# Performance work log

Measured on AMD Instinct MI355X. Metric: run time of the kernel, lower is better.

The kernel has to match this reference:

```python
import jax, jax.numpy as jnp
import numpy as np

DIM = 512
HEADS = 8
DH = DIM // HEADS          # 64
SCALE = DH ** (-0.5)
B, H, W = 8, 64, 64        # N = 4096, H and W multiples of 8 -> exact adaptive pool
N = H * W
POOL = 8                   # AdaptiveAvgPool2d((8,8)) -> 64 pooled tokens


def setup_inputs() -> dict:
    key = jax.random.key(0)
    ks = jax.random.split(key, 6)
    return {
        "x": jax.random.normal(ks[0], (B, N, DIM), dtype=jnp.float32),
        "proj_w": jax.random.normal(ks[1], (DIM, DIM), dtype=jnp.float32) * (DIM ** -0.5),
        "step_rep": jax.random.normal(ks[2], (HEADS, 1, 1), dtype=jnp.float32),
        "step_x": jax.random.normal(ks[3], (HEADS, 1, 1), dtype=jnp.float32),
        "to_out_w": jax.random.normal(ks[4], (DIM, DIM), dtype=jnp.float32) * (DIM ** -0.5),
        "to_out_b": jax.random.normal(ks[5], (DIM,), dtype=jnp.float32),
    }


def reference(x, proj_w, step_rep, step_x, to_out_w, to_out_b):
    b, n, c = x.shape
    # proj (Linear, no bias): w = x @ proj_w.T
    w = jnp.einsum('bnc,dc->bnd', x, proj_w)                       # [B,N,C]
    # AdaptiveAvgPool2d to (8,8): exact block mean since H,W % 8 == 0
    bh, bw = H // POOL, W // POOL
    rep = w.reshape(b, POOL, bh, POOL, bw, c).mean(axis=(2, 4))    # [B,8,8,C]
    rep = rep.reshape(b, POOL * POOL, c)                           # [B,64,C]
    # split heads: [B,h,tokens,dh]
    wh = w.reshape(b, n, HEADS, DH).transpose(0, 2, 1, 3)          # [B,h,N,dh]
    reph = rep.reshape(b, POOL * POOL, HEADS, DH).transpose(0, 2, 1, 3)  # [B,h,64,dh]
    # cross-attention: pooled queries vs full tokens (attn is reused later)
    dots = jnp.einsum('bhqd,bhkd->bhqk', reph, wh) * SCALE         # [B,h,64,N]
    attn = jax.nn.softmax(dots, axis=-1)
    rep_delta = jnp.einsum('bhqk,bhkd->bhqd', attn, wh)            # [B,h,64,dh]
    reph = reph + step_rep * rep_delta
    # self-attention among pooled reps
    dots2 = jnp.einsum('bhqd,bhkd->bhqk', reph, reph) * SCALE      # [B,h,64,64]
    attn2 = jax.nn.softmax(dots2, axis=-1)
    x_delta = jnp.einsum('bhqk,bhkd->bhqd', attn2, reph)           # [B,h,64,dh]
    # upsample back to tokens by reusing attn transposed
    x_delta = jnp.einsum('bhqn,bhqd->bhnd', attn, x_delta)         # [B,h,N,dh]
    x_delta = step_x * x_delta
    x_delta = x_delta.transpose(0, 2, 1, 3).reshape(b, n, c)       # [B,N,C]
    out = jnp.einsum('bnc,dc->bnd', x_delta, to_out_w) + to_out_b
    return out
```

## Files before the change

kernel.cpp:

```cpp
#include <hip/hip_runtime.h>
#include <hip/hip_bf16.h>
#include <stdint.h>

typedef __attribute__((ext_vector_type(8))) short short8v;
typedef __attribute__((ext_vector_type(4))) float floatx4;
typedef __attribute__((ext_vector_type(4))) unsigned uintx4;

#define DEV __device__ __forceinline__

DEV ushort f2bf(float f) {
  union { float f; unsigned u; } v; v.f = f;
  unsigned r = v.u + 0x7fffu + ((v.u >> 16) & 1u);
  return (ushort)(r >> 16);
}
DEV float bf2f(ushort b) {
  union { unsigned u; float f; } v; v.u = ((unsigned)b) << 16;
  return v.f;
}
DEV unsigned cvtpk(float lo, float hi) {
  unsigned r;
  asm("v_cvt_pk_bf16_f32 %0, %1, %2" : "=v"(r) : "v"(lo), "v"(hi));
  return r;
}
DEV int swz(int row, int colByte) {
  return row * 128 + (colByte ^ ((row & 7) << 4));
}
DEV int swz256(int row, int colByte) {
  return row * 256 + (colByte ^ ((row & 7) << 4));
}
DEV floatx4 mfma16(short8v a, short8v b, floatx4 c) {
  return __builtin_amdgcn_mfma_f32_16x16x32_bf16(a, b, c, 0, 0, 0);
}

#define GLD_LDS16(g, l)                                                   \
  __builtin_amdgcn_global_load_lds(                                       \
      (const __attribute__((address_space(1))) void*)(g),                 \
      (__attribute__((address_space(3))) void*)(l), 16, 0, 0)

constexpr int Bc = 8, HEADS = 8, NTOK = 4096, CDIM = 512, DH = 64;
constexpr float SCALE = 0.125f;
constexpr int NCH = 8, CHK = 512;

__global__ __launch_bounds__(256) void k_f2bfw(const float* __restrict__ a,
                                               const float* __restrict__ b,
                                               ushort* __restrict__ da,
                                               ushort* __restrict__ db) {
  int i = blockIdx.x * 256 + threadIdx.x;
  const float* s = (i < 65536) ? a : b;
  ushort* d = (i < 65536) ? da : db;
  int j = i & 65535;
  float4 f = ((const float4*)s)[j];
  ushort4 o;
  o.x = f2bf(f.x); o.y = f2bf(f.y); o.z = f2bf(f.z); o.w = f2bf(f.w);
  ((ushort4*)d)[j] = o;
}

__global__ __launch_bounds__(256) void k_gemm1f(const float* __restrict__ A,
                                                const ushort* __restrict__ Bm,
                                                ushort* __restrict__ Cout) {
  __shared__ ushort sA[128 * 64];
  __shared__ ushort sB[128 * 64];
  const int t = threadIdx.x;
  const int w = t >> 6, l = t & 63;
  const int lg = l >> 4, li = l & 15;
  const int bid = blockIdx.x;
  const int f = (bid & 7) * 128 + (bid >> 3);
  const int m0 = (f >> 2) * 128, n0 = (f & 3) * 128;
  const int wr = (w >> 1) * 64, wc = (w & 1) * 64;
  const int K = CDIM;
  floatx4 acc[4][4] = {};
#pragma unroll
  for (int kt = 0; kt < 8; ++kt) {
    float4 fa[4][2];
#pragma unroll
    for (int i = 0; i < 4; ++i) {
      int flat = i * 256 + t;
      int row = flat >> 3, pch = flat & 7;
      const float* ga = A + (size_t)(m0 + row) * K + kt * 64 + pch * 8;
      fa[i][0] = *(const float4*)ga;
      fa[i][1] = *(const float4*)(ga + 4);
    }
    __syncthreads();
#pragma unroll
    for (int i = 0; i < 4; ++i) {
      int flat = i * 256 + t;
      int row = flat >> 3, pch = flat & 7;
      int sch = pch ^ (row & 7);
      const ushort* gb = Bm + (size_t)(n0 + row) * K + kt * 64 + sch * 8;
      GLD_LDS16(gb, (char*)sB + flat * 16);
    }
#pragma unroll
    for (int i = 0; i < 4; ++i) {
      int flat = i * 256 + t;
      int row = flat >> 3, pch = flat & 7;
      uintx4 pk;
      pk.x = cvtpk(fa[i][0].x, fa[i][0].y);
      pk.y = cvtpk(fa[i][0].z, fa[i][0].w);
      pk.z = cvtpk(fa[i][1].x, fa[i][1].y);
      pk.w = cvtpk(fa[i][1].z, fa[i][1].w);
      *(uintx4*)((char*)sA + row * 128 + ((pch ^ (row & 7)) << 4)) = pk;
    }
    __syncthreads();
#pragma unroll
    for (int kk = 0; kk < 2; ++kk) {
      int colb = (kk * 32 + lg * 8) * 2;
      short8v af[4], bf[4];
#pragma unroll
      for (int m = 0; m < 4; ++m)
        af[m] = *(const short8v*)((const char*)sA + swz(wr + m * 16 + li, colb));
#pragma unroll
      for (int n = 0; n < 4; ++n)
        bf[n] = *(const short8v*)((const char*)sB + swz(wc + n * 16 + li, colb));
#pragma unroll
      for (int m = 0; m < 4; ++m)
#pragma unroll
        for (int n = 0; n < 4; ++n)
          acc[m][n] = mfma16(af[m], bf[n], acc[m][n]);
    }
  }
#pragma unroll
  for (int m = 0; m < 4; ++m)
#pragma unroll
    for (int n = 0; n < 4; ++n) {
      int col = n0 + wc + n * 16 + li;
#pragma unroll
      for (int r = 0; r < 4; ++r) {
        int row = m0 + wr + m * 16 + lg * 4 + r;
        Cout[(size_t)row * CDIM + col] = f2bf(acc[m][n][r]);
      }
    }
}

__global__ __launch_bounds__(256) void k_gemm3(const ushort* __restrict__ attnT,
                                               const ushort* __restrict__ M2T,
                                               float* __restrict__ out,
                                               const float* __restrict__ bias) {
  __shared__ ushort sA[128 * 64];
  __shared__ ushort sB[128 * 64];
  const int t = threadIdx.x;
  const int w = t >> 6, l = t & 63;
  const int lg = l >> 4, li = l & 15;
  const int bid = blockIdx.x;
  const int b = bid & 7;
  const int idx = bid >> 3;
  const int m0 = (idx >> 2) * 128, n0 = (idx & 3) * 128;
  const int wr = (w >> 1) * 64, wc = (w & 1) * 64;
  const ushort* Bb = M2T + (size_t)b * 262144;
  floatx4 acc[4][4] = {};
#pragma unroll
  for (int kt = 0; kt < 8; ++kt) {
    __syncthreads();
#pragma unroll
    for (int i = 0; i < 4; ++i) {
      int flat = i * 256 + t;
      int row = flat >> 3, pch = flat & 7;
      int sch = pch ^ (row & 7);
      const ushort* ga = attnT + (((size_t)(b * 8 + kt)) * NTOK + m0 + row) * 64 + sch * 8;
      GLD_LDS16(ga, (char*)sA + flat * 16);
    }
#pragma unroll
    for (int i = 0; i < 4; ++i) {
      int flat = i * 256 + t;
      int row = flat >> 3, pch = flat & 7;
      int sch = pch ^ (row & 7);
      const ushort* gb = Bb + (size_t)(n0 + row) * 512 + kt * 64 + sch * 8;
      GLD_LDS16(gb, (char*)sB + flat * 16);
    }
    __syncthreads();
#pragma unroll
    for (int kk = 0; kk < 2; ++kk) {
      int colb = (kk * 32 + lg * 8) * 2;
      short8v af[4], bf[4];
#pragma unroll
      for (int m = 0; m < 4; ++m)
        af[m] = *(const short8v*)((const char*)sA + swz(wr + m * 16 + li, colb));
#pragma unroll
      for (int n = 0; n < 4; ++n)
        bf[n] = *(const short8v*)((const char*)sB + swz(wc + n * 16 + li, colb));
#pragma unroll
      for (int m = 0; m < 4; ++m)
#pragma unroll
        for (int n = 0; n < 4; ++n)
          acc[m][n] = mfma16(af[m], bf[n], acc[m][n]);
    }
  }
#pragma unroll
  for (int m = 0; m < 4; ++m)
#pragma unroll
    for (int n = 0; n < 4; ++n) {
      int col = n0 + wc + n * 16 + li;
      float bv = bias[col];
#pragma unroll
      for (int r = 0; r < 4; ++r) {
        int row = m0 + wr + m * 16 + lg * 4 + r;
        out[((size_t)b * NTOK + row) * CDIM + col] = acc[m][n][r] + bv;
      }
    }
}

__global__ __launch_bounds__(256) void k_pool(const ushort* __restrict__ wm,
                                              float* __restrict__ rep,
                                              ushort* __restrict__ qbf) {
  const int blk = blockIdx.x;
  const int b = blk >> 6, qi = blk & 63;
  const int ph = qi >> 3, pw = qi & 7;
  const int c0 = threadIdx.x * 2;
  float a0 = 0.f, a1 = 0.f;
  for (int u = 0; u < 64; ++u) {
    int n = (ph * 8 + (u >> 3)) * 64 + pw * 8 + (u & 7);
    unsigned v = *(const unsigned*)(wm + ((size_t)b * NTOK + n) * CDIM + c0);
    a0 += bf2f((ushort)(v & 0xffff));
    a1 += bf2f((ushort)(v >> 16));
  }
  a0 *= 0.015625f; a1 *= 0.015625f;
  float* dst = rep + ((size_t)b * 64 + qi) * CDIM + c0;
  dst[0] = a0;
  dst[1] = a1;
  int h = c0 >> 6, d0 = c0 & 63;
  unsigned pack = (unsigned)f2bf(a0) | ((unsigned)f2bf(a1) << 16);
  *(unsigned*)((char*)qbf + ((size_t)(b * 8 + h)) * 8192 + swz(qi, d0 * 2)) = pack;
}

__global__ __launch_bounds__(256) void k_qkexp(const ushort* __restrict__ wmat,
                                               const ushort* __restrict__ qbf,
                                               ushort* __restrict__ attnT,
                                               float* __restrict__ pvP,
                                               float* __restrict__ rsumP) {
  __shared__ char smem[57344] __attribute__((aligned(128)));
  ushort* sQ  = (ushort*)smem;
  ushort* sK  = (ushort*)(smem + 8192);
  ushort* sVT = (ushort*)(smem + 24576);
  ushort* sP  = (ushort*)(smem + 40960);

  const int bh = blockIdx.y, ch = blockIdx.x;
  const int b = bh >> 3, h = bh & 7;
  const int t = threadIdx.x, w = t >> 6, l = t & 63;
  const int lg = l >> 4, li = l & 15;

  {
    const char* qsrc = (const char*)(qbf + (size_t)bh * 4096);
#pragma unroll
    for (int i = 0; i < 2; ++i) {
      int flat = i * 256 + t;
      GLD_LDS16(qsrc + flat * 16, (char*)sQ + flat * 16);
    }
  }

  float rs[4] = {};
  floatx4 pv[4] = {};
  short8v qa[2];
  bool qaLoaded = false;

  for (int sc = 0; sc < 4; ++sc) {
    const ushort* wbase = wmat + ((size_t)b * NTOK + ch * CHK + sc * 128) * CDIM + h * DH;
    __syncthreads();
#pragma unroll
    for (int i = 0; i < 4; ++i) {
      int flat = i * 256 + t;
      int row = flat >> 3, pch = flat & 7;
      int sch = pch ^ (row & 7);
      GLD_LDS16(wbase + (size_t)row * CDIM + sch * 8, (char*)sK + flat * 16);
    }
    {
      int u = t & 63;
      int dh2 = (t >> 6) * 16;
      const ushort* g0 = wbase + (size_t)(2 * u) * CDIM + dh2;
      const ushort* g1 = g0 + CDIM;
      short8v a0 = *(const short8v*)g0;
      short8v a1 = *(const short8v*)(g0 + 8);
      short8v b0 = *(const short8v*)g1;
      short8v b1 = *(const short8v*)(g1 + 8);
#pragma unroll
      for (int j = 0; j < 8; ++j) {
        unsigned w0 = ((unsigned)(ushort)a0[j]) | (((unsigned)(ushort)b0[j]) << 16);
        *(unsigned*)((char*)sVT + swz256(dh2 + j, 4 * u)) = w0;
        unsigned w1 = ((unsigned)(ushort)a1[j]) | (((unsigned)(ushort)b1[j]) << 16);
        *(unsigned*)((char*)sVT + swz256(dh2 + 8 + j, 4 * u)) = w1;
      }
    }
    __syncthreads();

    if (!qaLoaded) {
      qaLoaded = true;
#pragma unroll
      for (int kk = 0; kk < 2; ++kk)
        qa[kk] = *(const short8v*)((const char*)sQ + swz(w * 16 + li, (kk * 32 + lg * 8) * 2));
    }

    floatx4 s[8] = {};
#pragma unroll
    for (int kk = 0; kk < 2; ++kk) {
      int cb = (kk * 32 + lg * 8) * 2;
#pragma unroll
      for (int kf = 0; kf < 8; ++kf) {
        short8v kb = *(const short8v*)((const char*)sK + swz(kf * 16 + li, cb));
        s[kf] = mfma16(qa[kk], kb, s[kf]);
      }
    }

#pragma unroll
    for (int kf = 0; kf < 8; ++kf) {
      ushort pb[4];
#pragma unroll
      for (int r = 0; r < 4; ++r) {
        float p = __expf(s[kf][r] * SCALE);
        rs[r] += p;
        pb[r] = f2bf(p);
        int q = w * 16 + lg * 4 + r;
        *(ushort*)((char*)sP + swz256(q, (kf * 16 + li) * 2)) = pb[r];
      }
      int key = ch * CHK + sc * 128 + kf * 16 + li;
      ushort4 pk; pk.x = pb[0]; pk.y = pb[1]; pk.z = pb[2]; pk.w = pb[3];
      *(ushort4*)(attnT + ((size_t)bh * NTOK + key) * 64 + w * 16 + lg * 4) = pk;
    }

#pragma unroll
    for (int kk4 = 0; kk4 < 4; ++kk4) {
      int cb = kk4 * 64 + lg * 16;
      short8v pa = *(const short8v*)((const char*)sP + swz256(w * 16 + li, cb));
#pragma unroll
      for (int nf = 0; nf < 4; ++nf) {
        short8v vb = *(const short8v*)((const char*)sVT + swz256(nf * 16 + li, cb));
        pv[nf] = mfma16(pa, vb, pv[nf]);
      }
    }
  }

#pragma unroll
  for (int r = 0; r < 4; ++r) {
    float v = rs[r];
    for (int mask = 1; mask < 16; mask <<= 1) v += __shfl_xor(v, mask);
    if (li == 0) rsumP[((size_t)bh * NCH + ch) * 64 + w * 16 + lg * 4 + r] = v;
  }
  float* pvdst = pvP + ((size_t)bh * NCH + ch) * 4096;
#pragma unroll
  for (int nf = 0; nf < 4; ++nf)
#pragma unroll
    for (int r = 0; r < 4; ++r)
      pvdst[(w * 16 + lg * 4 + r) * 64 + nf * 16 + li] = pv[nf][r];
}

__global__ __launch_bounds__(256) void k_midm2(const float* __restrict__ rep,
                                               const float* __restrict__ pvP,
                                               const float* __restrict__ rsumP,
                                               const float* __restrict__ step_rep,
                                               const float* __restrict__ step_x,
                                               const ushort* __restrict__ tow,
                                               ushort* __restrict__ m2t) {
  __shared__ float sSum[64];
  __shared__ float sRd[4096];
  __shared__ float sR[64 * 65];
  __shared__ float sT[64 * 65];
  __shared__ ushort sXd[4096];
  const int bh = blockIdx.x;
  const int b = bh >> 3, h = bh & 7;
  const int t = threadIdx.x, w = t >> 6, l = t & 63;
  const int lg = l >> 4, li = l & 15;

  if (t < 64) {
    float v = 0.f;
#pragma unroll
    for (int ch = 0; ch < NCH; ++ch) v += rsumP[((size_t)bh * NCH + ch) * 64 + t];
    sSum[t] = v;
  }
  {
    const float* p = pvP + (size_t)bh * NCH * 4096;
#pragma unroll
    for (int j = 0; j < 16; ++j) {
      int idx = t + 256 * j;
      float sm = 0.f;
#pragma unroll
      for (int ch = 0; ch < NCH; ++ch) sm += p[ch * 4096 + idx];
      sRd[idx] = sm;
    }
  }
  __syncthreads();
  {
    int q = t >> 2, d0 = (t & 3) * 16;
    float srep = step_rep[h];
    float inv = 1.f / sSum[q];
    const float* rp = rep + ((size_t)b * 64 + q) * CDIM + h * DH + d0;
#pragma unroll
    for (int j = 0; j < 16; ++j) sR[q * 65 + d0 + j] = rp[j] + srep * (sRd[q * 64 + d0 + j] * inv);
  }
  __syncthreads();
  {
    int q = t >> 2, jb = (t & 3) * 16;
    float a[16];
#pragma unroll
    for (int j = 0; j < 16; ++j) {
      float accd = 0.f;
      for (int d = 0; d < 64; ++d) accd += sR[q * 65 + d] * sR[(jb + j) * 65 + d];
      a[j] = accd * SCALE;
    }
    float mx = a[0];
#pragma unroll
    for (int j = 1; j < 16; ++j) mx = fmaxf(mx, a[j]);
    mx = fmaxf(mx, __shfl_xor(mx, 1));
    mx = fmaxf(mx, __shfl_xor(mx, 2));
    float sm = 0.f;
#pragma unroll
    for (int j = 0; j < 16; ++j) { a[j] = __expf(a[j] - mx); sm += a[j]; }
    sm += __shfl_xor(sm, 1);
    sm += __shfl_xor(sm, 2);
    float inv = 1.f / sm;
#pragma unroll
    for (int j = 0; j < 16; ++j) sT[q * 65 + jb + j] = a[j] * inv;
  }
  __syncthreads();
  {
    int q = t >> 2, db = (t & 3) * 16;
    float accd[16] = {};
    for (int j = 0; j < 64; ++j) {
      float w2 = sT[q * 65 + j];
#pragma unroll
      for (int d = 0; d < 16; ++d) accd[d] += w2 * sR[j * 65 + db + d];
    }
    float sc = step_x[h] / sSum[q];
    ushort o[16] __attribute__((aligned(16)));
#pragma unroll
    for (int d = 0; d < 16; ++d) o[d] = f2bf(accd[d] * sc);
    *(short8v*)((char*)sXd + swz(q, db * 2)) = *(short8v*)&o[0];
    *(short8v*)((char*)sXd + swz(q, db * 2 + 16)) = *(short8v*)&o[8];
  }
  __syncthreads();
  floatx4 acc[8][4] = {};
#pragma unroll
  for (int kk = 0; kk < 2; ++kk) {
    int dd0 = kk * 32 + lg * 8;
    short8v bf[4];
#pragma unroll
    for (int nf = 0; nf < 4; ++nf)
      bf[nf] = *(const short8v*)((const char*)sXd + swz(nf * 16 + li, dd0 * 2));
#pragma unroll
    for (int m = 0; m < 8; ++m) {
      int d = w * 128 + m * 16 + li;
      short8v af = *(const short8v*)(tow + (size_t)d * CDIM + h * DH + dd0);
#pragma unroll
      for (int nf = 0; nf < 4; ++nf) acc[m][nf] = mfma16(af, bf[nf], acc[m][nf]);
    }
  }
#pragma unroll
  for (int m = 0; m < 8; ++m)
#pragma unroll
    for (int nf = 0; nf < 4; ++nf)
#pragma unroll
      for (int r = 0; r < 4; ++r) {
        int d = w * 128 + m * 16 + lg * 4 + r;
        int hq = h * 64 + nf * 16 + li;
        m2t[((size_t)b * CDIM + d) * CDIM + hq] = f2bf(acc[m][nf][r]);
      }
}

extern "C" void kernel_launch(void* const* d_in, const int* in_sizes, int n_in,
                              void* d_out, int out_size, void* d_ws, size_t ws_size,
                              hipStream_t stream) {
  const float* x = (const float*)d_in[0];
  const float* proj_w = (const float*)d_in[1];
  const float* step_rep = (const float*)d_in[2];
  const float* step_x = (const float*)d_in[3];
  const float* to_out_w = (const float*)d_in[4];
  const float* to_out_b = (const float*)d_in[5];
  float* out = (float*)d_out;
  char* ws = (char*)d_ws;
  char* ob = (char*)d_out;

  ushort* bufA = (ushort*)(ws);
  ushort* bufB = (ushort*)(ws + 33554432);
  ushort* pw   = (ushort*)(ws + 67108864);
  ushort* tow  = (ushort*)(ws + 67633152);
  float*  rep  = (float*)(ws + 68157440);
  float*  pvP   = (float*)(ob);
  ushort* qbf   = (ushort*)(ob + 34603008);
  float*  rsumP = (float*)(ob + 35127296);
  ushort* m2t   = bufB;

  k_f2bfw<<<512, 256, 0, stream>>>(proj_w, to_out_w, pw, tow);

  k_gemm1f<<<1024, 256, 0, stream>>>(x, pw, bufB);

  k_pool<<<Bc * 64, 256, 0, stream>>>(bufB, rep, qbf);

  k_qkexp<<<dim3(NCH, Bc * HEADS), 256, 0, stream>>>(bufB, qbf, bufA, pvP, rsumP);

  k_midm2<<<Bc * HEADS, 256, 0, stream>>>(rep, pvP, rsumP, step_rep, step_x, tow, m2t);

  k_gemm3<<<1024, 256, 0, stream>>>(bufA, m2t, out, to_out_b);
}
```

Measured before the change: 114.7 us.

## Double-buffer and enlarge GEMM tiles to 256x256 with register-staged prefetch

Both GEMM kernels move from 128x128 tiles with 256 threads to 256x256 tiles with 512 threads. Each block now double-buffers LDS and prefetches the next two k-tiles into registers, so global loads overlap MFMA work and each k-step needs one barrier instead of two. The direct global-to-LDS loads are replaced by register loads followed by swizzled LDS writes. The grid drops to 256 blocks, and the larger tiles raise register and LDS pressure, which may limit occupancy and leave some CUs idle.

Result: faster. 106.6 us (-7.1%).

```diff
diff --git a/kernel.cpp b/kernel.cpp
--- a/kernel.cpp
+++ b/kernel.cpp
@@ -36,6 +36,13 @@
   __builtin_amdgcn_global_load_lds(                                       \
       (const __attribute__((address_space(1))) void*)(g),                 \
       (__attribute__((address_space(3))) void*)(l), 16, 0, 0)
+
+#define WAIT_LGKM0 asm volatile("s_waitcnt lgkmcnt(0)" ::: "memory")
+DEV void sbar() {
+  __builtin_amdgcn_sched_barrier(0);
+  __builtin_amdgcn_s_barrier();
+  __builtin_amdgcn_sched_barrier(0);
+}
 
 constexpr int Bc = 8, HEADS = 8, NTOK = 4096, CDIM = 512, DH = 64;
 constexpr float SCALE = 0.125f;
@@ -55,71 +62,91 @@
   ((ushort4*)d)[j] = o;
 }
 
-__global__ __launch_bounds__(256) void k_gemm1f(const float* __restrict__ A,
-                                                const ushort* __restrict__ Bm,
-                                                ushort* __restrict__ Cout) {
-  __shared__ ushort sA[128 * 64];
-  __shared__ ushort sB[128 * 64];
+__global__ __launch_bounds__(512, 2) void k_gemm1(const float* __restrict__ A,
+                                                  const ushort* __restrict__ Bm,
+                                                  ushort* __restrict__ Cout) {
+  __shared__ ushort sA[2][256 * 64];
+  __shared__ ushort sB[2][256 * 64];
   const int t = threadIdx.x;
   const int w = t >> 6, l = t & 63;
   const int lg = l >> 4, li = l & 15;
   const int bid = blockIdx.x;
-  const int f = (bid & 7) * 128 + (bid >> 3);
-  const int m0 = (f >> 2) * 128, n0 = (f & 3) * 128;
-  const int wr = (w >> 1) * 64, wc = (w & 1) * 64;
-  const int K = CDIM;
-  floatx4 acc[4][4] = {};
+  const int f = (bid & 7) * 32 + (bid >> 3);
+  const int m0 = (f >> 1) * 256, n0 = (f & 1) * 256;
+  const int wr = (w >> 2) * 128, wc = (w & 3) * 64;
+
+  float4 fa[8];
+  short8v fb[4];
+
+  auto loadA = [&](int kt) {
+#pragma unroll
+    for (int i = 0; i < 4; ++i) {
+      int s = i * 512 + t, row = s >> 3, pch = s & 7;
+      const float* g = A + (size_t)(m0 + row) * CDIM + kt * 64 + pch * 8;
+      fa[2 * i] = *(const float4*)g;
+      fa[2 * i + 1] = *(const float4*)(g + 4);
+    }
+  };
+  auto loadB = [&](int kt) {
+#pragma unroll
+    for (int i = 0; i < 4; ++i) {
+      int s = i * 512 + t, row = s >> 3, pch = s & 7;
+      fb[i] = *(const short8v*)(Bm + (size_t)(n0 + row) * CDIM + kt * 64 + pch * 8);
+    }
+  };
+  auto writeAB = [&](int buf) {
+#pragma unroll
+    for (int i = 0; i < 4; ++i) {
+      int s = i * 512 + t, row = s >> 3, pch = s & 7;
+      int off = row * 128 + ((pch ^ (row & 7)) << 4);
+      uintx4 pk;
+      pk.x = cvtpk(fa[2 * i].x, fa[2 * i].y);
+      pk.y = cvtpk(fa[2 * i].z, fa[2 * i].w);
+      pk.z = cvtpk(fa[2 * i + 1].x, fa[2 * i + 1].y);
+      pk.w = cvtpk(fa[2 * i + 1].z, fa[2 * i + 1].w);
+      *(uintx4*)((char*)sA[buf] + off) = pk;
+      *(short8v*)((char*)sB[buf] + off) = fb[i];
+    }
+  };
+
+  floatx4 acc[8][4] = {};
+
+  loadA(0); loadB(0);
+  writeAB(0);
+  loadA(1); loadB(1);
+  WAIT_LGKM0;
+  sbar();
+
 #pragma unroll
   for (int kt = 0; kt < 8; ++kt) {
-    float4 fa[4][2];
-#pragma unroll
-    for (int i = 0; i < 4; ++i) {
-      int flat = i * 256 + t;
-      int row = flat >> 3, pch = flat & 7;
-      const float* ga = A + (size_t)(m0 + row) * K + kt * 64 + pch * 8;
-      fa[i][0] = *(const float4*)ga;
-      fa[i][1] = *(const float4*)(ga + 4);
-    }
-    __syncthreads();
-#pragma unroll
-    for (int i = 0; i < 4; ++i) {
-      int flat = i * 256 + t;
-      int row = flat >> 3, pch = flat & 7;
-      int sch = pch ^ (row & 7);
-      const ushort* gb = Bm + (size_t)(n0 + row) * K + kt * 64 + sch * 8;
-      GLD_LDS16(gb, (char*)sB + flat * 16);
-    }
-#pragma unroll
-    for (int i = 0; i < 4; ++i) {
-      int flat = i * 256 + t;
-      int row = flat >> 3, pch = flat & 7;
-      uintx4 pk;
-      pk.x = cvtpk(fa[i][0].x, fa[i][0].y);
-      pk.y = cvtpk(fa[i][0].z, fa[i][0].w);
-      pk.z = cvtpk(fa[i][1].x, fa[i][1].y);
-      pk.w = cvtpk(fa[i][1].z, fa[i][1].w);
-      *(uintx4*)((char*)sA + row * 128 + ((pch ^ (row & 7)) << 4)) = pk;
-    }
-    __syncthreads();
+    const int cur = kt & 1;
+    if (kt < 7) writeAB(cur ^ 1);
+    if (kt < 6) { loadA(kt + 2); loadB(kt + 2); }
 #pragma unroll
     for (int kk = 0; kk < 2; ++kk) {
       int colb = (kk * 32 + lg * 8) * 2;
-      short8v af[4], bf[4];
-#pragma unroll
-      for (int m = 0; m < 4; ++m)
-        af[m] = *(const short8v*)((const char*)sA + swz(wr + m * 16 + li, colb));
+      short8v bf[4];
 #pragma unroll
       for (int n = 0; n < 4; ++n)
-        bf[n] = *(const short8v*)((const char*)sB + swz(wc + n * 16 + li, colb));
-#pragma unroll
-      for (int m = 0; m < 4; ++m)
-#pragma unroll
-        for (int n = 0; n < 4; ++n)
-          acc[m][n] = mfma16(af[m], bf[n], acc[m][n]);
-    }
-  }
-#pragma unroll
-  for (int m = 0; m < 4; ++m)
+        bf[n] = *(const short8v*)((const char*)sB[cur] + swz(wc + n * 16 + li, colb));
+#pragma unroll
+      for (int mh = 0; mh < 2; ++mh) {
+        short8v af[4];
+#pragma unroll
+        for (int m = 0; m < 4; ++m)
+          af[m] = *(const short8v*)((const char*)sA[cur] + swz(wr + mh * 64 + m * 16 + li, colb));
+#pragma unroll
+        for (int m = 0; m < 4; ++m)
+#pragma unroll
+          for (int n = 0; n < 4; ++n)
+            acc[mh * 4 + m][n] = mfma16(af[m], bf[n], acc[mh * 4 + m][n]);
+      }
+    }
+    if (kt < 7) { WAIT_LGKM0; sbar(); }
+  }
+
+#pragma unroll
+  for (int m = 0; m < 8; ++m)
 #pragma unroll
     for (int n = 0; n < 4; ++n) {
       int col = n0 + wc + n * 16 + li;
@@ -131,61 +158,79 @@
     }
 }
 
-__global__ __launch_bounds__(256) void k_gemm3(const ushort* __restrict__ attnT,
-                                               const ushort* __restrict__ M2T,
-                                               float* __restrict__ out,
-                                               const float* __restrict__ bias) {
-  __shared__ ushort sA[128 * 64];
-  __shared__ ushort sB[128 * 64];
+__global__ __launch_bounds__(512, 2) void k_gemm3(const ushort* __restrict__ attnT,
+                                                  const ushort* __restrict__ M2T,
+                                                  float* __restrict__ out,
+                                                  const float* __restrict__ bias) {
+  __shared__ ushort sA[2][256 * 64];
+  __shared__ ushort sB[2][256 * 64];
   const int t = threadIdx.x;
   const int w = t >> 6, l = t & 63;
   const int lg = l >> 4, li = l & 15;
   const int bid = blockIdx.x;
   const int b = bid & 7;
   const int idx = bid >> 3;
-  const int m0 = (idx >> 2) * 128, n0 = (idx & 3) * 128;
-  const int wr = (w >> 1) * 64, wc = (w & 1) * 64;
+  const int m0 = (idx >> 1) * 256, n0 = (idx & 1) * 256;
+  const int wr = (w >> 2) * 128, wc = (w & 3) * 64;
   const ushort* Bb = M2T + (size_t)b * 262144;
-  floatx4 acc[4][4] = {};
+
+  short8v fA[4], fB[4];
+  auto loadAB = [&](int kt) {
+#pragma unroll
+    for (int i = 0; i < 4; ++i) {
+      int s = i * 512 + t, row = s >> 3, pch = s & 7;
+      fA[i] = *(const short8v*)(attnT + (((size_t)(b * 8 + kt)) * NTOK + m0 + row) * 64 + pch * 8);
+      fB[i] = *(const short8v*)(Bb + (size_t)(n0 + row) * CDIM + kt * 64 + pch * 8);
+    }
+  };
+  auto writeAB = [&](int buf) {
+#pragma unroll
+    for (int i = 0; i < 4; ++i) {
+      int s = i * 512 + t, row = s >> 3, pch = s & 7;
+      int off = row * 128 + ((pch ^ (row & 7)) << 4);
+      *(short8v*)((char*)sA[buf] + off) = fA[i];
+      *(short8v*)((char*)sB[buf] + off) = fB[i];
+    }
+  };
+
+  floatx4 acc[8][4] = {};
+
+  loadAB(0);
+  writeAB(0);
+  loadAB(1);
+  WAIT_LGKM0;
+  sbar();
+
 #pragma unroll
   for (int kt = 0; kt < 8; ++kt) {
-    __syncthreads();
-#pragma unroll
-    for (int i = 0; i < 4; ++i) {
-      int flat = i * 256 + t;
-      int row = flat >> 3, pch = flat & 7;
-      int sch = pch ^ (row & 7);
-      const ushort* ga = attnT + (((size_t)(b * 8 + kt)) * NTOK + m0 + row) * 64 + sch * 8;
-      GLD_LDS16(ga, (char*)sA + flat * 16);
-    }
-#pragma unroll
-    for (int i = 0; i < 4; ++i) {
-      int flat = i * 256 + t;
-      int row = flat >> 3, pch = flat & 7;
-      int sch = pch ^ (row & 7);
-      const ushort* gb = Bb + (size_t)(n0 + row) * 512 + kt * 64 + sch * 8;
-      GLD_LDS16(gb, (char*)sB + flat * 16);
-    }
-    __syncthreads();
+    const int cur = kt & 1;
+    if (kt < 7) writeAB(cur ^ 1);
+    if (kt < 6) loadAB(kt + 2);
 #pragma unroll
     for (int kk = 0; kk < 2; ++kk) {
       int colb = (kk * 32 + lg * 8) * 2;
-      short8v af[4], bf[4];
-#pragma unroll
-      for (int m = 0; m < 4; ++m)
-        af[m] = *(const short8v*)((const char*)sA + swz(wr + m * 16 + li, colb));
+      short8v bf[4];
 #pragma unroll
       for (int n = 0; n < 4; ++n)
-        bf[n] = *(const short8v*)((const char*)sB + swz(wc + n * 16 + li, colb));
-#pragma unroll
-      for (int m = 0; m < 4; ++m)
-#pragma unroll
-        for (int n = 0; n < 4; ++n)
-          acc[m][n] = mfma16(af[m], bf[n], acc[m][n]);
-    }
-  }
-#pragma unroll
-  for (int m = 0; m < 4; ++m)
+        bf[n] = *(const short8v*)((const char*)sB[cur] + swz(wc + n * 16 + li, colb));
+#pragma unroll
+      for (int mh = 0; mh < 2; ++mh) {
+        short8v af[4];
+#pragma unroll
+        for (int m = 0; m < 4; ++m)
+          af[m] = *(const short8v*)((const char*)sA[cur] + swz(wr + mh * 64 + m * 16 + li, colb));
+#pragma unroll
+        for (int m = 0; m < 4; ++m)
+#pragma unroll
+          for (int n = 0; n < 4; ++n)
+            acc[mh * 4 + m][n] = mfma16(af[m], bf[n], acc[mh * 4 + m][n]);
+      }
+    }
+    if (kt < 7) { WAIT_LGKM0; sbar(); }
+  }
+
+#pragma unroll
+  for (int m = 0; m < 8; ++m)
 #pragma unroll
     for (int n = 0; n < 4; ++n) {
       int col = n0 + wc + n * 16 + li;
@@ -477,7 +522,7 @@
 
   k_f2bfw<<<512, 256, 0, stream>>>(proj_w, to_out_w, pw, tow);
 
-  k_gemm1f<<<1024, 256, 0, stream>>>(x, pw, bufB);
+  k_gemm1<<<256, 512, 0, stream>>>(x, pw, bufB);
 
   k_pool<<<Bc * 64, 256, 0, stream>>>(bufB, rep, qbf);
 
@@ -485,5 +530,5 @@
 
   k_midm2<<<Bc * HEADS, 256, 0, stream>>>(rep, pvP, rsumP, step_rep, step_x, tow, m2t);
 
-  k_gemm3<<<1024, 256, 0, stream>>>(bufA, m2t, out, to_out_b);
-}
+  k_gemm3<<<256, 512, 0, stream>>>(bufA, m2t, out, to_out_b);
+}
```

## Triple-buffer async global-to-LDS loads in both projection GEMMs

Applied to the files above, without the earlier changes.

Both GEMM kernels now use a three-stage LDS ring filled with asynchronous global_load_lds, with K-steps of 32 and explicit vmcnt waits, so loads for later tiles overlap MFMA work on the current tile. The first GEMM stages raw fp32 x tiles in LDS and converts them to bf16 when reading fragments, instead of loading into registers and converting before the LDS store. This removes one barrier per step and the register round-trip. In exchange it uses more LDS per block (72KB and 48KB), which can reduce occupancy, and the smaller K-step doubles the number of barriers.

After: 119.7 us. 4.4% more time.

```diff
diff --git a/kernel.cpp b/kernel.cpp
--- a/kernel.cpp
+++ b/kernel.cpp
@@ -25,6 +25,9 @@
 DEV int swz(int row, int colByte) {
   return row * 128 + (colByte ^ ((row & 7) << 4));
 }
+DEV int swz64(int row, int colByte) {
+  return row * 64 + (colByte ^ ((row & 3) << 4));
+}
 DEV int swz256(int row, int colByte) {
   return row * 256 + (colByte ^ ((row & 7) << 4));
 }
@@ -36,6 +39,15 @@
   __builtin_amdgcn_global_load_lds(                                       \
       (const __attribute__((address_space(1))) void*)(g),                 \
       (__attribute__((address_space(3))) void*)(l), 16, 0, 0)
+
+#define WAITVM6 asm volatile("s_waitcnt vmcnt(6)" ::: "memory")
+#define WAITVM4 asm volatile("s_waitcnt vmcnt(4)" ::: "memory")
+#define WAITVM0 asm volatile("s_waitcnt vmcnt(0)" ::: "memory")
+DEV void barrier_seq() {
+  __builtin_amdgcn_sched_barrier(0);
+  __builtin_amdgcn_s_barrier();
+  __builtin_amdgcn_sched_barrier(0);
+}
 
 constexpr int Bc = 8, HEADS = 8, NTOK = 4096, CDIM = 512, DH = 64;
 constexpr float SCALE = 0.125f;
@@ -55,11 +67,10 @@
   ((ushort4*)d)[j] = o;
 }
 
-__global__ __launch_bounds__(256) void k_gemm1f(const float* __restrict__ A,
-                                                const ushort* __restrict__ Bm,
-                                                ushort* __restrict__ Cout) {
-  __shared__ ushort sA[128 * 64];
-  __shared__ ushort sB[128 * 64];
+__global__ __launch_bounds__(256, 2) void k_gemm1(const float* __restrict__ A,
+                                                  const ushort* __restrict__ Bm,
+                                                  ushort* __restrict__ Cout) {
+  __shared__ char smem[73728] __attribute__((aligned(128)));
   const int t = threadIdx.x;
   const int w = t >> 6, l = t & 63;
   const int lg = l >> 4, li = l & 15;
@@ -67,57 +78,56 @@
   const int f = (bid & 7) * 128 + (bid >> 3);
   const int m0 = (f >> 2) * 128, n0 = (f & 3) * 128;
   const int wr = (w >> 1) * 64, wc = (w & 1) * 64;
-  const int K = CDIM;
+
+  auto issue = [&](int kt) {
+    char* sa = smem + (kt % 3) * 24576;
+    char* sb = sa + 16384;
+#pragma unroll
+    for (int i = 0; i < 4; ++i) {
+      int flat = i * 256 + t, row = flat >> 3, pch = flat & 7;
+      int sch = pch ^ (row & 7);
+      GLD_LDS16(A + (size_t)(m0 + row) * CDIM + kt * 32 + sch * 4, sa + flat * 16);
+    }
+#pragma unroll
+    for (int i = 0; i < 2; ++i) {
+      int flat = i * 256 + t, row = flat >> 2, pch = flat & 3;
+      int sch = pch ^ (row & 3);
+      GLD_LDS16(Bm + (size_t)(n0 + row) * CDIM + kt * 32 + sch * 8, sb + flat * 16);
+    }
+  };
+
   floatx4 acc[4][4] = {};
-#pragma unroll
-  for (int kt = 0; kt < 8; ++kt) {
-    float4 fa[4][2];
-#pragma unroll
-    for (int i = 0; i < 4; ++i) {
-      int flat = i * 256 + t;
-      int row = flat >> 3, pch = flat & 7;
-      const float* ga = A + (size_t)(m0 + row) * K + kt * 64 + pch * 8;
-      fa[i][0] = *(const float4*)ga;
-      fa[i][1] = *(const float4*)(ga + 4);
-    }
-    __syncthreads();
-#pragma unroll
-    for (int i = 0; i < 4; ++i) {
-      int flat = i * 256 + t;
-      int row = flat >> 3, pch = flat & 7;
-      int sch = pch ^ (row & 7);
-      const ushort* gb = Bm + (size_t)(n0 + row) * K + kt * 64 + sch * 8;
-      GLD_LDS16(gb, (char*)sB + flat * 16);
-    }
-#pragma unroll
-    for (int i = 0; i < 4; ++i) {
-      int flat = i * 256 + t;
-      int row = flat >> 3, pch = flat & 7;
-      uintx4 pk;
-      pk.x = cvtpk(fa[i][0].x, fa[i][0].y);
-      pk.y = cvtpk(fa[i][0].z, fa[i][0].w);
-      pk.z = cvtpk(fa[i][1].x, fa[i][1].y);
-      pk.w = cvtpk(fa[i][1].z, fa[i][1].w);
-      *(uintx4*)((char*)sA + row * 128 + ((pch ^ (row & 7)) << 4)) = pk;
-    }
-    __syncthreads();
-#pragma unroll
-    for (int kk = 0; kk < 2; ++kk) {
-      int colb = (kk * 32 + lg * 8) * 2;
-      short8v af[4], bf[4];
-#pragma unroll
-      for (int m = 0; m < 4; ++m)
-        af[m] = *(const short8v*)((const char*)sA + swz(wr + m * 16 + li, colb));
+  issue(0);
+  issue(1);
+
+#pragma unroll
+  for (int kt = 0; kt < 16; ++kt) {
+    if (kt < 15) { WAITVM6; } else { WAITVM0; }
+    barrier_seq();
+    if (kt + 2 < 16) issue(kt + 2);
+    const char* sa = smem + (kt % 3) * 24576;
+    const char* sb = sa + 16384;
+    short8v af[4], bf[4];
+#pragma unroll
+    for (int m = 0; m < 4; ++m) {
+      int row = wr + m * 16 + li;
+      float4 lo = *(const float4*)(sa + swz(row, lg * 32));
+      float4 hi = *(const float4*)(sa + swz(row, lg * 32 + 16));
+      uintx4 u;
+      u.x = cvtpk(lo.x, lo.y); u.y = cvtpk(lo.z, lo.w);
+      u.z = cvtpk(hi.x, hi.y); u.w = cvtpk(hi.z, hi.w);
+      af[m] = *(short8v*)&u;
+    }
+#pragma unroll
+    for (int n = 0; n < 4; ++n)
+      bf[n] = *(const short8v*)(sb + swz64(wc + n * 16 + li, lg * 16));
+#pragma unroll
+    for (int m = 0; m < 4; ++m)
 #pragma unroll
       for (int n = 0; n < 4; ++n)
-        bf[n] = *(const short8v*)((const char*)sB + swz(wc + n * 16 + li, colb));
-#pragma unroll
-      for (int m = 0; m < 4; ++m)
-#pragma unroll
-        for (int n = 0; n < 4; ++n)
-          acc[m][n] = mfma16(af[m], bf[n], acc[m][n]);
-    }
-  }
+        acc[m][n] = mfma16(af[m], bf[n], acc[m][n]);
+  }
+
 #pragma unroll
   for (int m = 0; m < 4; ++m)
 #pragma unroll
@@ -131,12 +141,11 @@
     }
 }
 
-__global__ __launch_bounds__(256) void k_gemm3(const ushort* __restrict__ attnT,
-                                               const ushort* __restrict__ M2T,
-                                               float* __restrict__ out,
-                                               const float* __restrict__ bias) {
-  __shared__ ushort sA[128 * 64];
-  __shared__ ushort sB[128 * 64];
+__global__ __launch_bounds__(256, 3) void k_gemm3(const ushort* __restrict__ attnT,
+                                                  const ushort* __restrict__ M2T,
+                                                  float* __restrict__ out,
+                                                  const float* __restrict__ bias) {
+  __shared__ char smem[49152] __attribute__((aligned(128)));
   const int t = threadIdx.x;
   const int w = t >> 6, l = t & 63;
   const int lg = l >> 4, li = l & 15;
@@ -146,44 +155,51 @@
   const int m0 = (idx >> 2) * 128, n0 = (idx & 3) * 128;
   const int wr = (w >> 1) * 64, wc = (w & 1) * 64;
   const ushort* Bb = M2T + (size_t)b * 262144;
+
+  auto issue = [&](int kt) {
+    char* sa = smem + (kt % 3) * 16384;
+    char* sb = sa + 8192;
+    int h = kt >> 1, qh = (kt & 1) * 32;
+#pragma unroll
+    for (int i = 0; i < 2; ++i) {
+      int flat = i * 256 + t, row = flat >> 2, pch = flat & 3;
+      int sch = pch ^ (row & 3);
+      GLD_LDS16(attnT + (((size_t)(b * 8 + h)) * NTOK + m0 + row) * 64 + qh + sch * 8,
+                sa + flat * 16);
+    }
+#pragma unroll
+    for (int i = 0; i < 2; ++i) {
+      int flat = i * 256 + t, row = flat >> 2, pch = flat & 3;
+      int sch = pch ^ (row & 3);
+      GLD_LDS16(Bb + (size_t)(n0 + row) * CDIM + kt * 32 + sch * 8, sb + flat * 16);
+    }
+  };
+
   floatx4 acc[4][4] = {};
-#pragma unroll
-  for (int kt = 0; kt < 8; ++kt) {
-    __syncthreads();
-#pragma unroll
-    for (int i = 0; i < 4; ++i) {
-      int flat = i * 256 + t;
-      int row = flat >> 3, pch = flat & 7;
-      int sch = pch ^ (row & 7);
-      const ushort* ga = attnT + (((size_t)(b * 8 + kt)) * NTOK + m0 + row) * 64 + sch * 8;
-      GLD_LDS16(ga, (char*)sA + flat * 16);
-    }
-#pragma unroll
-    for (int i = 0; i < 4; ++i) {
-      int flat = i * 256 + t;
-      int row = flat >> 3, pch = flat & 7;
-      int sch = pch ^ (row & 7);
-      const ushort* gb = Bb + (size_t)(n0 + row) * 512 + kt * 64 + sch * 8;
-      GLD_LDS16(gb, (char*)sB + flat * 16);
-    }
-    __syncthreads();
-#pragma unroll
-    for (int kk = 0; kk < 2; ++kk) {
-      int colb = (kk * 32 + lg * 8) * 2;
-      short8v af[4], bf[4];
-#pragma unroll
-      for (int m = 0; m < 4; ++m)
-        af[m] = *(const short8v*)((const char*)sA + swz(wr + m * 16 + li, colb));
+  issue(0);
+  issue(1);
+
+#pragma unroll
+  for (int kt = 0; kt < 16; ++kt) {
+    if (kt < 15) { WAITVM4; } else { WAITVM0; }
+    barrier_seq();
+    if (kt + 2 < 16) issue(kt + 2);
+    const char* sa = smem + (kt % 3) * 16384;
+    const char* sb = sa + 8192;
+    short8v af[4], bf[4];
+#pragma unroll
+    for (int m = 0; m < 4; ++m)
+      af[m] = *(const short8v*)(sa + swz64(wr + m * 16 + li, lg * 16));
+#pragma unroll
+    for (int n = 0; n < 4; ++n)
+      bf[n] = *(const short8v*)(sb + swz64(wc + n * 16 + li, lg * 16));
+#pragma unroll
+    for (int m = 0; m < 4; ++m)
 #pragma unroll
       for (int n = 0; n < 4; ++n)
-        bf[n] = *(const short8v*)((const char*)sB + swz(wc + n * 16 + li, colb));
-#pragma unroll
-      for (int m = 0; m < 4; ++m)
-#pragma unroll
-        for (int n = 0; n < 4; ++n)
-          acc[m][n] = mfma16(af[m], bf[n], acc[m][n]);
-    }
-  }
+        acc[m][n] = mfma16(af[m], bf[n], acc[m][n]);
+  }
+
 #pragma unroll
   for (int m = 0; m < 4; ++m)
 #pragma unroll
@@ -477,7 +493,7 @@
 
   k_f2bfw<<<512, 256, 0, stream>>>(proj_w, to_out_w, pw, tow);
 
-  k_gemm1f<<<1024, 256, 0, stream>>>(x, pw, bufB);
+  k_gemm1<<<1024, 256, 0, stream>>>(x, pw, bufB);
 
   k_pool<<<Bc * 64, 256, 0, stream>>>(bufB, rep, qbf);
 
```

## Restructure GEMMs to keep full-K B tile resident in LDS with register-streamed A

Applied to the files above, without the earlier changes.

Both large GEMMs now stage the entire 128x512 bf16 B panel into 128KB of LDS once per block, then stream A directly from global into registers with one-step prefetch. Each block handles a 512-row strip in two passes with 512 threads at one block per CU. This removes per-k-tile LDS staging and barriers for A. The to_out_w bf16 conversion is dropped, and k_midm2 converts the fp32 weights inline instead. The cost is lower occupancy (one block per CU, 256 blocks) and uncoalesced-ish direct global A loads.

After: 124.7 us. 1.09x slower.

```diff
diff --git a/kernel.cpp b/kernel.cpp
--- a/kernel.cpp
+++ b/kernel.cpp
@@ -41,161 +41,143 @@
 constexpr float SCALE = 0.125f;
 constexpr int NCH = 8, CHK = 512;
 
-__global__ __launch_bounds__(256) void k_f2bfw(const float* __restrict__ a,
-                                               const float* __restrict__ b,
-                                               ushort* __restrict__ da,
-                                               ushort* __restrict__ db) {
-  int i = blockIdx.x * 256 + threadIdx.x;
-  const float* s = (i < 65536) ? a : b;
-  ushort* d = (i < 65536) ? da : db;
-  int j = i & 65535;
-  float4 f = ((const float4*)s)[j];
+__global__ __launch_bounds__(256) void k_f2bfw1(const float* __restrict__ a,
+                                                ushort* __restrict__ da) {
+  int j = blockIdx.x * 256 + threadIdx.x;
+  float4 f = ((const float4*)a)[j];
   ushort4 o;
   o.x = f2bf(f.x); o.y = f2bf(f.y); o.z = f2bf(f.z); o.w = f2bf(f.w);
-  ((ushort4*)d)[j] = o;
-}
-
-__global__ __launch_bounds__(256) void k_gemm1f(const float* __restrict__ A,
-                                                const ushort* __restrict__ Bm,
-                                                ushort* __restrict__ Cout) {
-  __shared__ ushort sA[128 * 64];
-  __shared__ ushort sB[128 * 64];
-  const int t = threadIdx.x;
-  const int w = t >> 6, l = t & 63;
+  ((ushort4*)da)[j] = o;
+}
+
+DEV void stageB(const ushort* __restrict__ Bsrc, int n0, char* sB, int t) {
+#pragma unroll
+  for (int i = 0; i < 16; ++i) {
+    int flat = i * 512 + t;
+    int n = flat >> 6, c = flat & 63;
+    int sc = (c & ~7) | ((c & 7) ^ (n & 7));
+    GLD_LDS16(Bsrc + (size_t)(n0 + n) * CDIM + sc * 8, sB + flat * 16);
+  }
+}
+DEV short8v readB(const char* sB, int n, int gc) {
+  int c = (gc & ~7) | ((gc & 7) ^ (n & 7));
+  return *(const short8v*)(sB + n * 1024 + c * 16);
+}
+
+__global__ __launch_bounds__(512, 1) void k_gemm1(const float* __restrict__ A,
+                                                  const ushort* __restrict__ Bm,
+                                                  ushort* __restrict__ Cout) {
+  __shared__ char sB[131072] __attribute__((aligned(128)));
+  const int t = threadIdx.x, w = t >> 6, l = t & 63;
   const int lg = l >> 4, li = l & 15;
   const int bid = blockIdx.x;
-  const int f = (bid & 7) * 128 + (bid >> 3);
-  const int m0 = (f >> 2) * 128, n0 = (f & 3) * 128;
-  const int wr = (w >> 1) * 64, wc = (w & 1) * 64;
-  const int K = CDIM;
-  floatx4 acc[4][4] = {};
-#pragma unroll
-  for (int kt = 0; kt < 8; ++kt) {
-    float4 fa[4][2];
-#pragma unroll
-    for (int i = 0; i < 4; ++i) {
-      int flat = i * 256 + t;
-      int row = flat >> 3, pch = flat & 7;
-      const float* ga = A + (size_t)(m0 + row) * K + kt * 64 + pch * 8;
-      fa[i][0] = *(const float4*)ga;
-      fa[i][1] = *(const float4*)(ga + 4);
-    }
-    __syncthreads();
-#pragma unroll
-    for (int i = 0; i < 4; ++i) {
-      int flat = i * 256 + t;
-      int row = flat >> 3, pch = flat & 7;
-      int sch = pch ^ (row & 7);
-      const ushort* gb = Bm + (size_t)(n0 + row) * K + kt * 64 + sch * 8;
-      GLD_LDS16(gb, (char*)sB + flat * 16);
-    }
-#pragma unroll
-    for (int i = 0; i < 4; ++i) {
-      int flat = i * 256 + t;
-      int row = flat >> 3, pch = flat & 7;
-      uintx4 pk;
-      pk.x = cvtpk(fa[i][0].x, fa[i][0].y);
-      pk.y = cvtpk(fa[i][0].z, fa[i][0].w);
-      pk.z = cvtpk(fa[i][1].x, fa[i][1].y);
-      pk.w = cvtpk(fa[i][1].z, fa[i][1].w);
-      *(uintx4*)((char*)sA + row * 128 + ((pch ^ (row & 7)) << 4)) = pk;
-    }
-    __syncthreads();
-#pragma unroll
-    for (int kk = 0; kk < 2; ++kk) {
-      int colb = (kk * 32 + lg * 8) * 2;
-      short8v af[4], bf[4];
-#pragma unroll
-      for (int m = 0; m < 4; ++m)
-        af[m] = *(const short8v*)((const char*)sA + swz(wr + m * 16 + li, colb));
-#pragma unroll
-      for (int n = 0; n < 4; ++n)
-        bf[n] = *(const short8v*)((const char*)sB + swz(wc + n * 16 + li, colb));
-#pragma unroll
-      for (int m = 0; m < 4; ++m)
-#pragma unroll
-        for (int n = 0; n < 4; ++n)
-          acc[m][n] = mfma16(af[m], bf[n], acc[m][n]);
-    }
-  }
-#pragma unroll
-  for (int m = 0; m < 4; ++m)
-#pragma unroll
-    for (int n = 0; n < 4; ++n) {
-      int col = n0 + wc + n * 16 + li;
-#pragma unroll
-      for (int r = 0; r < 4; ++r) {
-        int row = m0 + wr + m * 16 + lg * 4 + r;
-        Cout[(size_t)row * CDIM + col] = f2bf(acc[m][n][r]);
-      }
-    }
-}
-
-__global__ __launch_bounds__(256) void k_gemm3(const ushort* __restrict__ attnT,
-                                               const ushort* __restrict__ M2T,
-                                               float* __restrict__ out,
-                                               const float* __restrict__ bias) {
-  __shared__ ushort sA[128 * 64];
-  __shared__ ushort sB[128 * 64];
-  const int t = threadIdx.x;
-  const int w = t >> 6, l = t & 63;
+  const int xcd = bid & 7, loc = bid >> 3;
+  const int strip = xcd * 8 + (loc >> 2);
+  const int n0 = (loc & 3) * 128;
+
+  stageB(Bm, n0, sB, t);
+  __syncthreads();
+
+#pragma unroll
+  for (int pass = 0; pass < 2; ++pass) {
+    const size_t r0 = (size_t)strip * 512 + pass * 256 + w * 32;
+    floatx4 acc[2][8] = {};
+    const float* ga0 = A + (r0 + li) * CDIM + lg * 8;
+    const float* ga1 = A + (r0 + 16 + li) * CDIM + lg * 8;
+    float4 c00 = *(const float4*)ga0, c01 = *(const float4*)(ga0 + 4);
+    float4 c10 = *(const float4*)ga1, c11 = *(const float4*)(ga1 + 4);
+#pragma unroll
+    for (int kt = 0; kt < 16; ++kt) {
+      float4 n00, n01, n10, n11;
+      if (kt < 15) {
+        const float* g0 = ga0 + (kt + 1) * 32;
+        const float* g1 = ga1 + (kt + 1) * 32;
+        n00 = *(const float4*)g0; n01 = *(const float4*)(g0 + 4);
+        n10 = *(const float4*)g1; n11 = *(const float4*)(g1 + 4);
+      }
+      uintx4 u0, u1;
+      u0.x = cvtpk(c00.x, c00.y); u0.y = cvtpk(c00.z, c00.w);
+      u0.z = cvtpk(c01.x, c01.y); u0.w = cvtpk(c01.z, c01.w);
+      u1.x = cvtpk(c10.x, c10.y); u1.y = cvtpk(c10.z, c10.w);
+      u1.z = cvtpk(c11.x, c11.y); u1.w = cvtpk(c11.z, c11.w);
+      short8v a0 = *(short8v*)&u0, a1 = *(short8v*)&u1;
+#pragma unroll
+      for (int nf = 0; nf < 8; ++nf) {
+        short8v bf = readB(sB, nf * 16 + li, kt * 4 + lg);
+        acc[0][nf] = mfma16(a0, bf, acc[0][nf]);
+        acc[1][nf] = mfma16(a1, bf, acc[1][nf]);
+      }
+      c00 = n00; c01 = n01; c10 = n10; c11 = n11;
+    }
+#pragma unroll
+    for (int mi = 0; mi < 2; ++mi)
+#pragma unroll
+      for (int nf = 0; nf < 8; ++nf)
+#pragma unroll
+        for (int r = 0; r < 4; ++r) {
+          size_t row = r0 + mi * 16 + lg * 4 + r;
+          Cout[row * CDIM + n0 + nf * 16 + li] = f2bf(acc[mi][nf][r]);
+        }
+  }
+}
+
+__global__ __launch_bounds__(512, 1) void k_gemm3(const ushort* __restrict__ attnT,
+                                                  const ushort* __restrict__ M2T,
+                                                  float* __restrict__ out,
+                                                  const float* __restrict__ bias) {
+  __shared__ char sB[131072] __attribute__((aligned(128)));
+  const int t = threadIdx.x, w = t >> 6, l = t & 63;
   const int lg = l >> 4, li = l & 15;
   const int bid = blockIdx.x;
-  const int b = bid & 7;
-  const int idx = bid >> 3;
-  const int m0 = (idx >> 2) * 128, n0 = (idx & 3) * 128;
-  const int wr = (w >> 1) * 64, wc = (w & 1) * 64;
-  const ushort* Bb = M2T + (size_t)b * 262144;
-  floatx4 acc[4][4] = {};
-#pragma unroll
-  for (int kt = 0; kt < 8; ++kt) {
-    __syncthreads();
-#pragma unroll
-    for (int i = 0; i < 4; ++i) {
-      int flat = i * 256 + t;
-      int row = flat >> 3, pch = flat & 7;
-      int sch = pch ^ (row & 7);
-      const ushort* ga = attnT + (((size_t)(b * 8 + kt)) * NTOK + m0 + row) * 64 + sch * 8;
-      GLD_LDS16(ga, (char*)sA + flat * 16);
-    }
-#pragma unroll
-    for (int i = 0; i < 4; ++i) {
-      int flat = i * 256 + t;
-      int row = flat >> 3, pch = flat & 7;
-      int sch = pch ^ (row & 7);
-      const ushort* gb = Bb + (size_t)(n0 + row) * 512 + kt * 64 + sch * 8;
-      GLD_LDS16(gb, (char*)sB + flat * 16);
-    }
-    __syncthreads();
-#pragma unroll
-    for (int kk = 0; kk < 2; ++kk) {
-      int colb = (kk * 32 + lg * 8) * 2;
-      short8v af[4], bf[4];
-#pragma unroll
-      for (int m = 0; m < 4; ++m)
-        af[m] = *(const short8v*)((const char*)sA + swz(wr + m * 16 + li, colb));
-#pragma unroll
-      for (int n = 0; n < 4; ++n)
-        bf[n] = *(const short8v*)((const char*)sB + swz(wc + n * 16 + li, colb));
-#pragma unroll
-      for (int m = 0; m < 4; ++m)
-#pragma unroll
-        for (int n = 0; n < 4; ++n)
-          acc[m][n] = mfma16(af[m], bf[n], acc[m][n]);
-    }
-  }
-#pragma unroll
-  for (int m = 0; m < 4; ++m)
-#pragma unroll
-    for (int n = 0; n < 4; ++n) {
-      int col = n0 + wc + n * 16 + li;
-      float bv = bias[col];
-#pragma unroll
-      for (int r = 0; r < 4; ++r) {
-        int row = m0 + wr + m * 16 + lg * 4 + r;
-        out[((size_t)b * NTOK + row) * CDIM + col] = acc[m][n][r] + bv;
-      }
-    }
+  const int b = bid & 7, loc = bid >> 3;
+  const int strip = loc >> 2;
+  const int n0 = (loc & 3) * 128;
+
+  stageB(M2T + (size_t)b * 262144, n0, sB, t);
+  __syncthreads();
+
+#pragma unroll
+  for (int pass = 0; pass < 2; ++pass) {
+    const int r0 = strip * 512 + pass * 256 + w * 32;
+    floatx4 acc[2][8] = {};
+    const char* gaBase = (const char*)(attnT + (size_t)b * 8 * NTOK * 64);
+    short8v cA0, cA1;
+    {
+      const char* g = gaBase + (size_t)(r0 + li) * 128 + lg * 16;
+      cA0 = *(const short8v*)g;
+      cA1 = *(const short8v*)(g + 16 * 128);
+    }
+#pragma unroll
+    for (int kt = 0; kt < 16; ++kt) {
+      short8v nA0, nA1;
+      if (kt < 15) {
+        int k1 = kt + 1;
+        const char* g = gaBase + ((size_t)(k1 >> 1) * NTOK + r0 + li) * 128 +
+                        (k1 & 1) * 64 + lg * 16;
+        nA0 = *(const short8v*)g;
+        nA1 = *(const short8v*)(g + 16 * 128);
+      }
+#pragma unroll
+      for (int nf = 0; nf < 8; ++nf) {
+        short8v bf = readB(sB, nf * 16 + li, kt * 4 + lg);
+        acc[0][nf] = mfma16(cA0, bf, acc[0][nf]);
+        acc[1][nf] = mfma16(cA1, bf, acc[1][nf]);
+      }
+      cA0 = nA0; cA1 = nA1;
+    }
+#pragma unroll
+    for (int mi = 0; mi < 2; ++mi)
+#pragma unroll
+      for (int nf = 0; nf < 8; ++nf) {
+        int col = n0 + nf * 16 + li;
+        float bv = bias[col];
+#pragma unroll
+        for (int r = 0; r < 4; ++r) {
+          int row = r0 + mi * 16 + lg * 4 + r;
+          out[((size_t)b * NTOK + row) * CDIM + col] = acc[mi][nf][r] + bv;
+        }
+      }
+  }
 }
 
 __global__ __launch_bounds__(256) void k_pool(const ushort* __restrict__ wm,
@@ -345,7 +327,7 @@
                                                const float* __restrict__ rsumP,
                                                const float* __restrict__ step_rep,
                                                const float* __restrict__ step_x,
-                                               const ushort* __restrict__ tow,
+                                               const float* __restrict__ tow,
                                                ushort* __restrict__ m2t) {
   __shared__ float sSum[64];
   __shared__ float sRd[4096];
@@ -435,7 +417,13 @@
 #pragma unroll
     for (int m = 0; m < 8; ++m) {
       int d = w * 128 + m * 16 + li;
-      short8v af = *(const short8v*)(tow + (size_t)d * CDIM + h * DH + dd0);
+      const float* g = tow + (size_t)d * CDIM + h * DH + dd0;
+      float4 lo = *(const float4*)g;
+      float4 hi = *(const float4*)(g + 4);
+      uintx4 u;
+      u.x = cvtpk(lo.x, lo.y); u.y = cvtpk(lo.z, lo.w);
+      u.z = cvtpk(hi.x, hi.y); u.w = cvtpk(hi.z, hi.w);
+      short8v af = *(short8v*)&u;
 #pragma unroll
       for (int nf = 0; nf < 4; ++nf) acc[m][nf] = mfma16(af, bf[nf], acc[m][nf]);
     }
@@ -468,22 +456,21 @@
   ushort* bufA = (ushort*)(ws);
   ushort* bufB = (ushort*)(ws + 33554432);
   ushort* pw   = (ushort*)(ws + 67108864);
-  ushort* tow  = (ushort*)(ws + 67633152);
   float*  rep  = (float*)(ws + 68157440);
   float*  pvP   = (float*)(ob);
   ushort* qbf   = (ushort*)(ob + 34603008);
   float*  rsumP = (float*)(ob + 35127296);
   ushort* m2t   = bufB;
 
-  k_f2bfw<<<512, 256, 0, stream>>>(proj_w, to_out_w, pw, tow);
-
-  k_gemm1f<<<1024, 256, 0, stream>>>(x, pw, bufB);
+  k_f2bfw1<<<256, 256, 0, stream>>>(proj_w, pw);
+
+  k_gemm1<<<256, 512, 0, stream>>>(x, pw, bufB);
 
   k_pool<<<Bc * 64, 256, 0, stream>>>(bufB, rep, qbf);
 
   k_qkexp<<<dim3(NCH, Bc * HEADS), 256, 0, stream>>>(bufB, qbf, bufA, pvP, rsumP);
 
-  k_midm2<<<Bc * HEADS, 256, 0, stream>>>(rep, pvP, rsumP, step_rep, step_x, tow, m2t);
-
-  k_gemm3<<<1024, 256, 0, stream>>>(bufA, m2t, out, to_out_b);
-}
+  k_midm2<<<Bc * HEADS, 256, 0, stream>>>(rep, pvP, rsumP, step_rep, step_x, to_out_w, m2t);
+
+  k_gemm3<<<256, 512, 0, stream>>>(bufA, m2t, out, to_out_b);
+}
```
